# Optimization experiments

Hardware: AMD Instinct MI355X
Metric: run time of the kernel (lower is better)

The kernel has to match this reference:

```python
import jax, jax.numpy as jnp
import numpy as np

B, S, D_IN, D_OUT = 4, 2048, 1024, 1024


def setup_inputs() -> dict:
    key = jax.random.key(0)
    k1, k2, k3, k4 = jax.random.split(key, 4)
    scale = 1.0 / np.sqrt(D_IN)
    return {
        "x": jax.random.normal(k1, (B, S, D_IN), dtype=jnp.float32),
        "W_q": jax.random.normal(k2, (D_OUT, D_IN), dtype=jnp.float32) * scale,
        "W_k": jax.random.normal(k3, (D_OUT, D_IN), dtype=jnp.float32) * scale,
        "W_v": jax.random.normal(k4, (D_OUT, D_IN), dtype=jnp.float32) * scale,
    }


def reference(x, W_q, W_k, W_v):
    # torch nn.Linear: y = x @ W.T (bias=False)
    q = jnp.einsum("bsd,od->bso", x, W_q)
    k = jnp.einsum("bsd,od->bso", x, W_k)
    v = jnp.einsum("bsd,od->bso", x, W_v)
    s = q.shape[1]
    scores = jnp.einsum("bqo,bko->bqk", q, k)  # [B, S, S]
    causal = jnp.triu(jnp.ones((s, s), dtype=bool), k=1)
    scores = jnp.where(causal, -jnp.inf, scores)
    inv_sqrt_d = 1.0 / jnp.sqrt(jnp.asarray(q.shape[-1], scores.dtype))
    attn = jax.nn.softmax(scores * inv_sqrt_d, axis=-1)
    # dropout p=0.0 -> identity (deterministic reference)
    return jnp.einsum("bqk,bko->bqo", attn, v)
```

## Files before the change

### kernel.cpp

```cpp
#include <hip/hip_runtime.h>

typedef unsigned short u16;
typedef __bf16 bf16x8 __attribute__((ext_vector_type(8)));
typedef float f32x4 __attribute__((ext_vector_type(4)));

#define AS1 __attribute__((address_space(1)))
#define AS3 __attribute__((address_space(3)))

__device__ inline u16 f2bf(float f) {
  union { float f; unsigned u; } a; a.f = f;
  unsigned u = a.u;
  return (u16)((u + 0x7fffu + ((u >> 16) & 1u)) >> 16);
}

__global__ __launch_bounds__(256) void cvt_all_kernel(
    const float* __restrict__ x, const float* __restrict__ wq,
    const float* __restrict__ wk, const float* __restrict__ wv,
    u16* __restrict__ xb, u16* __restrict__ wqb,
    u16* __restrict__ wkb, u16* __restrict__ wvb) {
  int bid = blockIdx.x;
  const float* in; u16* out;
  if (bid < 8192) { in = x; out = xb; }
  else if (bid < 9216) { in = wq; out = wqb; bid -= 8192; }
  else if (bid < 10240) { in = wk; out = wkb; bid -= 9216; }
  else { in = wv; out = wvb; bid -= 10240; }
  size_t i = ((size_t)bid * 256 + threadIdx.x) * 4;
  float4 v = *(const float4*)(in + i);
  ushort4 o;
  o.x = f2bf(v.x); o.y = f2bf(v.y); o.z = f2bf(v.z); o.w = f2bf(v.w);
  *(ushort4*)(out + i) = o;
}

template <typename CT, int BN>
__device__ __forceinline__ void gemm_core(
    u16* __restrict__ lds,
    const u16* __restrict__ A, const u16* __restrict__ B, CT* __restrict__ C,
    int nt, int lda, int ldb, int ldc, int m0, int n0) {
  constexpr int ABUF = 16384;
  constexpr int BBUF = BN * 64;
  constexpr int BSW = BN / 64;
  constexpr int NI = BN / 64;

  const int tid = threadIdx.x;
  const int ln = tid & 63, wv = tid >> 6;
  const int wr = wv >> 2, wc = wv & 3;

  auto sweep = [&](const u16* src, int ld, int t, int s, int base) {
    const int c = s * 512 + tid;
    const int row = c >> 3, slot = c & 7;
    const int col = (slot ^ (row & 7)) * 8;
    __builtin_amdgcn_global_load_lds(
        (const AS1 void*)(src + (size_t)row * ld + (size_t)t * 64 + col),
        (AS3 void*)(&lds[base + c * 8]), 16, 0, 0);
  };

  f32x4 acc[8][NI] = {};

#pragma unroll
  for (int s = 0; s < BSW; ++s) sweep(B, ldb, 0, s, 2 * ABUF);
#pragma unroll
  for (int s = 0; s < 4; ++s) sweep(A, lda, 0, s, 0);
  if (nt > 1) {
#pragma unroll
    for (int s = 0; s < BSW; ++s) sweep(B, ldb, 1, s, 2 * ABUF + BBUF);
#pragma unroll
    for (int s = 0; s < 4; ++s) sweep(A, lda, 1, s, ABUF);
    if constexpr (BSW == 4) asm volatile("s_waitcnt vmcnt(8)" ::: "memory");
    else                    asm volatile("s_waitcnt vmcnt(6)" ::: "memory");
  } else {
    asm volatile("s_waitcnt vmcnt(0)" ::: "memory");
  }
  __builtin_amdgcn_s_barrier();

  for (int t = 0; t < nt; ++t) {
    const int p = t & 1;
    const u16* La = &lds[p * ABUF];
    const u16* Lb = &lds[2 * ABUF + p * BBUF];
    bf16x8 bfr[NI][2];
#pragma unroll
    for (int q = 0; q < 4; ++q) {
      if (q == 0) {
        __builtin_amdgcn_sched_barrier(0);
#pragma unroll
        for (int ni = 0; ni < NI; ++ni)
#pragma unroll
          for (int ks = 0; ks < 2; ++ks) {
            const int row = wc * (BN / 4) + ni * 16 + (ln & 15);
            const int kc = ks * 4 + (ln >> 4);
            bfr[ni][ks] = *(const bf16x8*)&Lb[row * 64 + ((kc ^ (row & 7)) << 3)];
          }
      }
      bf16x8 afr[2][2];
#pragma unroll
      for (int mi = 0; mi < 2; ++mi)
#pragma unroll
        for (int ks = 0; ks < 2; ++ks) {
          const int row = wr * 128 + (q * 2 + mi) * 16 + (ln & 15);
          const int kc = ks * 4 + (ln >> 4);
          afr[mi][ks] = *(const bf16x8*)&La[row * 64 + ((kc ^ (row & 7)) << 3)];
        }
      if (q == 0)      { if (t >= 1 && t + 1 < nt) { sweep(A, lda, t + 1, 0, (p ^ 1) * ABUF); sweep(A, lda, t + 1, 1, (p ^ 1) * ABUF); } }
      else if (q == 1) { if (t >= 1 && t + 1 < nt) { sweep(A, lda, t + 1, 2, (p ^ 1) * ABUF); sweep(A, lda, t + 1, 3, (p ^ 1) * ABUF); } }
      else if (q == 2) { if (t + 2 < nt) { sweep(B, ldb, t + 2, 0, 2 * ABUF + p * BBUF); if (BSW == 4) sweep(B, ldb, t + 2, 1, 2 * ABUF + p * BBUF); } }
      else             { if (t + 2 < nt) { if (BSW == 4) { sweep(B, ldb, t + 2, 2, 2 * ABUF + p * BBUF); sweep(B, ldb, t + 2, 3, 2 * ABUF + p * BBUF); } else { sweep(B, ldb, t + 2, 1, 2 * ABUF + p * BBUF); } } }

      __builtin_amdgcn_s_barrier();
      __builtin_amdgcn_s_setprio(1);
#pragma unroll
      for (int mi = 0; mi < 2; ++mi)
#pragma unroll
        for (int ni = 0; ni < NI; ++ni)
#pragma unroll
          for (int ks = 0; ks < 2; ++ks)
            acc[q * 2 + mi][ni] = __builtin_amdgcn_mfma_f32_16x16x32_bf16(
                afr[mi][ks], bfr[ni][ks], acc[q * 2 + mi][ni], 0, 0, 0);
      __builtin_amdgcn_s_setprio(0);
      if (q == 3) {
        if (t + 2 < nt) {
          if constexpr (BSW == 4) asm volatile("s_waitcnt vmcnt(4)" ::: "memory");
          else                    asm volatile("s_waitcnt vmcnt(2)" ::: "memory");
        } else if (t + 1 < nt) {
          asm volatile("s_waitcnt vmcnt(0)" ::: "memory");
        }
      }
      __builtin_amdgcn_s_barrier();
    }
  }

#pragma unroll
  for (int mi = 0; mi < 8; ++mi) {
    const int rbase = m0 + wr * 128 + mi * 16 + (ln >> 4) * 4;
#pragma unroll
    for (int ni = 0; ni < NI; ++ni) {
      const int col = n0 + wc * (BN / 4) + ni * 16 + (ln & 15);
#pragma unroll
      for (int r = 0; r < 4; ++r) {
        const float v = acc[mi][ni][r];
        CT* ptr = &C[(size_t)(rbase + r) * ldc + col];
        if constexpr (sizeof(CT) == 4) *(float*)ptr = v;
        else                           *ptr = f2bf(v);
      }
    }
  }
}

__global__ __launch_bounds__(512, 2) void proj_qk_kernel(
    const u16* __restrict__ xb, const u16* __restrict__ wqb,
    const u16* __restrict__ wkb, u16* __restrict__ Qb, u16* __restrict__ Kb) {
  __shared__ __align__(16) u16 lds[65536];
  const int bid = blockIdx.x;
  const int w = bid >> 7, r = bid & 127;
  const int rb = r >> 2, n0 = (r & 3) * 256;
  const u16* B = w ? wkb : wqb;
  u16* C = w ? Kb : Qb;
  gemm_core<u16, 256>(lds, xb + (size_t)rb * 256 * 1024, B + (size_t)n0 * 1024,
                      C, 16, 1024, 1024, 1024, rb * 256, n0);
}

__global__ __launch_bounds__(512, 2) void qktvt_kernel(
    const u16* __restrict__ Qb, const u16* __restrict__ Kb, float* __restrict__ Sb,
    const u16* __restrict__ wvb, const u16* __restrict__ xb, u16* __restrict__ VTb) {
  __shared__ __align__(16) u16 lds[65536];
  const int bid = blockIdx.x;
  if (bid < 144) {
    const int z = bid / 36, xt = bid % 36;
    int m = 0;
    while ((m + 1) * (m + 2) / 2 <= xt) ++m;
    const int n = xt - m * (m + 1) / 2;
    gemm_core<float, 256>(lds,
        Qb + ((size_t)z * 2048 + m * 256) * 1024,
        Kb + ((size_t)z * 2048 + n * 256) * 1024,
        Sb + (size_t)z * 2048 * 2048,
        16, 1024, 1024, 2048, m * 256, n * 256);
  } else {
    const int j = bid - 144;
    const int z = j / 28, r2 = j % 28, d = r2 / 7, kb = r2 % 7;
    gemm_core<u16, 256>(lds, wvb + (size_t)d * 256 * 1024,
                        xb + (size_t)z * 2048 * 1024 + (size_t)kb * 256 * 1024,
                        VTb + (size_t)z * 1024 * 2048,
                        16, 1024, 1024, 2048, d * 256, kb * 256);
  }
}

__global__ __launch_bounds__(512, 2) void smvtk_kernel(
    float* __restrict__ Sb,
    const u16* __restrict__ wvb, const u16* __restrict__ xb) {
  __shared__ __align__(16) u16 lds[65536];
  const int bid = blockIdx.x;
  const int tid = threadIdx.x;
  if (bid < 64) {
    const int z = bid >> 4, r = bid & 15;
    const int d = r >> 2, kf = (r >> 1) & 1, h = r & 1;
    const u16* A = wvb + (size_t)d * 256 * 1024 + h * 512;
    const u16* B = xb + ((size_t)z * 2048 + 1792 + kf * 128) * 1024 + h * 512;
    const int i = (d * 2 + kf) * 2 + h;
    const int band = i >> 3, coli = i & 7;
    float* C = Sb + (size_t)z * 2048 * 2048 + (size_t)band * 256 * 2048 +
               1024 + coli * 128;
    gemm_core<float, 128>(lds, A, B, C, 8, 1024, 1024, 2048, 0, 0);
    return;
  }
  const int j = bid - 64;
  const int m = 7 - (j >> 6), z = (j >> 4) & 3, s = j & 15;
  const int iters = m + 1;
  const int wvid = tid >> 6, lane = tid & 63;
  float* S0 = Sb + (size_t)z * 2048 * 2048;
  for (int rr = wvid; rr < 16; rr += 8) {
    const int r = m * 256 + s * 16 + rr;
    float* row = S0 + (size_t)r * 2048;
    float vals[8][4];
    float mx = -3.4e38f;
#pragma unroll
    for (int it2 = 0; it2 < 8; ++it2)
      if (it2 < iters) {
        const int idx = it2 * 64 + lane;
        float4 v = ((const float4*)row)[idx];
        const int j0 = idx * 4;
        vals[it2][0] = (j0 <= r) ? v.x * 0.03125f : -3.4e38f;
        vals[it2][1] = (j0 + 1 <= r) ? v.y * 0.03125f : -3.4e38f;
        vals[it2][2] = (j0 + 2 <= r) ? v.z * 0.03125f : -3.4e38f;
        vals[it2][3] = (j0 + 3 <= r) ? v.w * 0.03125f : -3.4e38f;
        mx = fmaxf(mx, fmaxf(fmaxf(vals[it2][0], vals[it2][1]),
                             fmaxf(vals[it2][2], vals[it2][3])));
      }
#pragma unroll
    for (int o = 32; o; o >>= 1) mx = fmaxf(mx, __shfl_xor(mx, o, 64));
    float sum = 0.f;
#pragma unroll
    for (int it2 = 0; it2 < 8; ++it2)
      if (it2 < iters) {
#pragma unroll
        for (int e = 0; e < 4; ++e) {
          const float pp = __expf(vals[it2][e] - mx);
          vals[it2][e] = pp;
          sum += pp;
        }
      }
#pragma unroll
    for (int o = 32; o; o >>= 1) sum += __shfl_xor(sum, o, 64);
    const float rcp = 1.f / sum;
    u16* prow = (u16*)row;
#pragma unroll
    for (int it2 = 0; it2 < 8; ++it2)
      if (it2 < iters) {
        ushort4 o4;
        o4.x = f2bf(vals[it2][0] * rcp);
        o4.y = f2bf(vals[it2][1] * rcp);
        o4.z = f2bf(vals[it2][2] * rcp);
        o4.w = f2bf(vals[it2][3] * rcp);
        ((ushort4*)prow)[it2 * 64 + lane] = o4;
      }
  }
}

__global__ __launch_bounds__(256) void vtfix_kernel(const float* __restrict__ Sb,
                                                    u16* __restrict__ VTb) {
  const int bid = blockIdx.x;
  const int z = bid >> 3, sdk = bid & 7;
  const int d = sdk >> 1, kf = sdk & 1;
  const int i0 = sdk * 2;
  const int band = i0 >> 3, coli = i0 & 7;
  const float* P0 = Sb + (size_t)z * 2048 * 2048 + (size_t)band * 256 * 2048 +
                    1024 + coli * 128;
  const float* P1 = P0 + 128;
  u16* dst = VTb + (size_t)z * 1024 * 2048 + (size_t)d * 256 * 2048 +
             1792 + kf * 128;
  for (int k = threadIdx.x; k < 8192; k += 256) {
    const int r = k >> 5, c4 = (k & 31) << 2;
    float4 a = *(const float4*)(P0 + (size_t)r * 2048 + c4);
    float4 b = *(const float4*)(P1 + (size_t)r * 2048 + c4);
    ushort4 o;
    o.x = f2bf(a.x + b.x); o.y = f2bf(a.y + b.y);
    o.z = f2bf(a.z + b.z); o.w = f2bf(a.w + b.w);
    *(ushort4*)(dst + (size_t)r * 2048 + c4) = o;
  }
}

__constant__ signed char CPM[16] = {5,5,7,7,7,6,4,4,6,6,3,3,1,2,2,0};
__constant__ signed char CPK[16] = {0,12,0,11,22,0,0,10,10,19,0,8,0,0,6,0};
__constant__ signed char CPN[16] = {12,12,11,11,10,10,10,10,9,9,8,8,8,6,6,4};
__constant__ signed char CPS[16] = {0,1,0,1,2,0,0,1,1,2,0,1,0,0,1,0};

__global__ __launch_bounds__(512, 2) void pv_kernel(
    const u16* __restrict__ P, const u16* __restrict__ VTb,
    float* __restrict__ out, float* __restrict__ Sb) {
  __shared__ __align__(16) u16 lds[65536];
  const int cls = blockIdx.x, n = blockIdx.y;
  const size_t z = blockIdx.z;
  const int m = CPM[cls], k0 = CPK[cls], ntc = CPN[cls], sl = CPS[cls];
  const u16* Ap = P + z * 2048 * 4096 + (size_t)m * 256 * 4096 + (size_t)k0 * 64;
  const u16* Bp = VTb + z * 1024 * 2048 + (size_t)n * 256 * 2048 + (size_t)k0 * 64;
  float* Cp;
  int ldc;
  if (sl == 0) { Cp = out + z * 2048 * 1024; ldc = 1024; }
  else if (sl == 1) { Cp = Sb + z * 2048 * 2048 + 1024; ldc = 2048; }
  else { Cp = Sb + z * 2048 * 2048 + 1024 - (size_t)1536 * 2048; ldc = 2048; }
  gemm_core<float, 256>(lds, Ap, Bp, Cp, ntc, 4096, 2048, ldc, m * 256, n * 256);
}

__global__ __launch_bounds__(256) void reduce_kernel(float* __restrict__ out,
                                                     const float* __restrict__ Sb) {
  const int j = blockIdx.x;
  const int m = 2 + (j >> 5), z = (j >> 3) & 3, s = j & 7;
  float* ob = out + (size_t)z * 2048 * 1024;
  const float* s1 = Sb + (size_t)z * 2048 * 2048 + 1024;
  const float* s2 = s1 - (size_t)1536 * 2048;
  const int r0 = m * 256 + s * 32;
  for (int k = threadIdx.x; k < 32 * 256; k += 256) {
    const int rr = r0 + (k >> 8), cc = k & 255;
    float4 o = ((float4*)(ob + (size_t)rr * 1024))[cc];
    float4 a = ((const float4*)(s1 + (size_t)rr * 2048))[cc];
    o.x += a.x; o.y += a.y; o.z += a.z; o.w += a.w;
    if (m >= 6) {
      float4 b = ((const float4*)(s2 + (size_t)rr * 2048))[cc];
      o.x += b.x; o.y += b.y; o.z += b.z; o.w += b.w;
    }
    ((float4*)(ob + (size_t)rr * 1024))[cc] = o;
  }
}

extern "C" void kernel_launch(void* const* d_in, const int* in_sizes, int n_in,
                              void* d_out, int out_size, void* d_ws, size_t ws_size,
                              hipStream_t stream) {
  const float* x  = (const float*)d_in[0];
  const float* Wq = (const float*)d_in[1];
  const float* Wk = (const float*)d_in[2];
  const float* Wv = (const float*)d_in[3];
  float* out = (float*)d_out;

  char* ws = (char*)d_ws;
  u16* xb   = (u16*)(ws);
  u16* wqb  = (u16*)(ws + (16ul << 20));
  u16* wkb  = (u16*)(ws + (18ul << 20));
  u16* wvb  = (u16*)(ws + (20ul << 20));
  u16* Qb   = (u16*)(ws + (22ul << 20));
  u16* Kb   = (u16*)(ws + (38ul << 20));
  u16* VTb  = (u16*)(ws + (54ul << 20));
  float* Sb = (float*)(ws + (70ul << 20));

  cvt_all_kernel<<<11264, 256, 0, stream>>>(x, Wq, Wk, Wv, xb, wqb, wkb, wvb);

  proj_qk_kernel<<<256, 512, 0, stream>>>(xb, wqb, wkb, Qb, Kb);

  qktvt_kernel<<<256, 512, 0, stream>>>(Qb, Kb, Sb, wvb, xb, VTb);

  smvtk_kernel<<<576, 512, 0, stream>>>(Sb, wvb, xb);

  vtfix_kernel<<<32, 256, 0, stream>>>(Sb, VTb);

  pv_kernel<<<dim3(16, 4, 4), 512, 0, stream>>>((const u16*)Sb, VTb, out, Sb);

  reduce_kernel<<<192, 256, 0, stream>>>(out, Sb);
}
```

Before: 172.7 us.

## Store attention scores in bf16 and move split-K partials to a separate buffer

The QK^T GEMM now writes its scores as bf16 instead of fp32, and the softmax pass reads and writes those bf16 values in place, which halves score-matrix traffic. The partial sums for the V^T tail and the PV split-K results move from scratch space inside the score buffer to a dedicated buffer R with new addressing. The qktvt block order is also interleaved so that score tiles and V^T tiles mix across the grid. The cost is that scores are rounded to bf16 before softmax, which lowers precision.

```diff
diff --git a/kernel.cpp b/kernel.cpp
--- a/kernel.cpp
+++ b/kernel.cpp
@@ -1,6 +1,7 @@
 #include <hip/hip_runtime.h>
 
 typedef unsigned short u16;
+typedef unsigned int u32;
 typedef __bf16 bf16x8 __attribute__((ext_vector_type(8)));
 typedef float f32x4 __attribute__((ext_vector_type(4)));
 
@@ -11,6 +12,9 @@
   union { float f; unsigned u; } a; a.f = f;
   unsigned u = a.u;
   return (u16)((u + 0x7fffu + ((u >> 16) & 1u)) >> 16);
+}
+__device__ inline float bf2f(u16 h) {
+  union { unsigned u; float f; } a; a.u = ((u32)h) << 16; return a.f;
 }
 
 __global__ __launch_bounds__(256) void cvt_all_kernel(
@@ -158,22 +162,23 @@
 }
 
 __global__ __launch_bounds__(512, 2) void qktvt_kernel(
-    const u16* __restrict__ Qb, const u16* __restrict__ Kb, float* __restrict__ Sb,
+    const u16* __restrict__ Qb, const u16* __restrict__ Kb, u16* __restrict__ Sb16,
     const u16* __restrict__ wvb, const u16* __restrict__ xb, u16* __restrict__ VTb) {
   __shared__ __align__(16) u16 lds[65536];
   const int bid = blockIdx.x;
-  if (bid < 144) {
-    const int z = bid / 36, xt = bid % 36;
+  const int item = (bid & 7) * 32 + (bid >> 3);
+  if (item < 144) {
+    const int z = item / 36, xt = item % 36;
     int m = 0;
     while ((m + 1) * (m + 2) / 2 <= xt) ++m;
     const int n = xt - m * (m + 1) / 2;
-    gemm_core<float, 256>(lds,
+    gemm_core<u16, 256>(lds,
         Qb + ((size_t)z * 2048 + m * 256) * 1024,
         Kb + ((size_t)z * 2048 + n * 256) * 1024,
-        Sb + (size_t)z * 2048 * 2048,
+        Sb16 + (size_t)z * 2048 * 2048,
         16, 1024, 1024, 2048, m * 256, n * 256);
   } else {
-    const int j = bid - 144;
+    const int j = item - 144;
     const int z = j / 28, r2 = j % 28, d = r2 / 7, kb = r2 % 7;
     gemm_core<u16, 256>(lds, wvb + (size_t)d * 256 * 1024,
                         xb + (size_t)z * 2048 * 1024 + (size_t)kb * 256 * 1024,
@@ -182,55 +187,53 @@
   }
 }
 
-__global__ __launch_bounds__(512, 2) void smvtk_kernel(
-    float* __restrict__ Sb,
+__global__ __launch_bounds__(512, 2) void smvt_kernel(
+    u16* __restrict__ Sb16, float* __restrict__ R,
     const u16* __restrict__ wvb, const u16* __restrict__ xb) {
   __shared__ __align__(16) u16 lds[65536];
   const int bid = blockIdx.x;
   const int tid = threadIdx.x;
-  if (bid < 64) {
-    const int z = bid >> 4, r = bid & 15;
-    const int d = r >> 2, kf = (r >> 1) & 1, h = r & 1;
+  if (bid < 32) {
+    const int z = bid >> 3, r = bid & 7;
+    const int d = r >> 1, h = r & 1;
     const u16* A = wvb + (size_t)d * 256 * 1024 + h * 512;
-    const u16* B = xb + ((size_t)z * 2048 + 1792 + kf * 128) * 1024 + h * 512;
-    const int i = (d * 2 + kf) * 2 + h;
-    const int band = i >> 3, coli = i & 7;
-    float* C = Sb + (size_t)z * 2048 * 2048 + (size_t)band * 256 * 2048 +
-               1024 + coli * 128;
-    gemm_core<float, 128>(lds, A, B, C, 8, 1024, 1024, 2048, 0, 0);
+    const u16* B = xb + ((size_t)z * 2048 + 1792) * 1024 + h * 512;
+    float* C = R + (size_t)z * 2097152 + 1572864 + (d * 2 + h) * 65536;
+    gemm_core<float, 256>(lds, A, B, C, 8, 1024, 1024, 256, 0, 0);
     return;
   }
-  const int j = bid - 64;
+  const int j = bid - 32;
   const int m = 7 - (j >> 6), z = (j >> 4) & 3, s = j & 15;
-  const int iters = m + 1;
+  const int iters = (m + 2) >> 1;
   const int wvid = tid >> 6, lane = tid & 63;
-  float* S0 = Sb + (size_t)z * 2048 * 2048;
+  u16* S0 = Sb16 + (size_t)z * 2048 * 2048;
   for (int rr = wvid; rr < 16; rr += 8) {
     const int r = m * 256 + s * 16 + rr;
-    float* row = S0 + (size_t)r * 2048;
-    float vals[8][4];
+    u16* row = S0 + (size_t)r * 2048;
+    float vals[4][8];
     float mx = -3.4e38f;
 #pragma unroll
-    for (int it2 = 0; it2 < 8; ++it2)
+    for (int it2 = 0; it2 < 4; ++it2)
       if (it2 < iters) {
-        const int idx = it2 * 64 + lane;
-        float4 v = ((const float4*)row)[idx];
-        const int j0 = idx * 4;
-        vals[it2][0] = (j0 <= r) ? v.x * 0.03125f : -3.4e38f;
-        vals[it2][1] = (j0 + 1 <= r) ? v.y * 0.03125f : -3.4e38f;
-        vals[it2][2] = (j0 + 2 <= r) ? v.z * 0.03125f : -3.4e38f;
-        vals[it2][3] = (j0 + 3 <= r) ? v.w * 0.03125f : -3.4e38f;
-        mx = fmaxf(mx, fmaxf(fmaxf(vals[it2][0], vals[it2][1]),
-                             fmaxf(vals[it2][2], vals[it2][3])));
+        const int idx8 = it2 * 512 + lane * 8;
+        uint4 w = *(const uint4*)(row + idx8);
+        const u32 ws[4] = {w.x, w.y, w.z, w.w};
+#pragma unroll
+        for (int e = 0; e < 8; ++e) {
+          const u16 hb = (u16)(ws[e >> 1] >> ((e & 1) * 16));
+          const float xv = bf2f(hb) * 0.03125f;
+          vals[it2][e] = (idx8 + e <= r) ? xv : -3.4e38f;
+          mx = fmaxf(mx, vals[it2][e]);
+        }
       }
 #pragma unroll
     for (int o = 32; o; o >>= 1) mx = fmaxf(mx, __shfl_xor(mx, o, 64));
     float sum = 0.f;
 #pragma unroll
-    for (int it2 = 0; it2 < 8; ++it2)
+    for (int it2 = 0; it2 < 4; ++it2)
       if (it2 < iters) {
 #pragma unroll
-        for (int e = 0; e < 4; ++e) {
+        for (int e = 0; e < 8; ++e) {
           const float pp = __expf(vals[it2][e] - mx);
           vals[it2][e] = pp;
           sum += pp;
@@ -239,40 +242,40 @@
 #pragma unroll
     for (int o = 32; o; o >>= 1) sum += __shfl_xor(sum, o, 64);
     const float rcp = 1.f / sum;
-    u16* prow = (u16*)row;
-#pragma unroll
-    for (int it2 = 0; it2 < 8; ++it2)
+#pragma unroll
+    for (int it2 = 0; it2 < 4; ++it2)
       if (it2 < iters) {
-        ushort4 o4;
-        o4.x = f2bf(vals[it2][0] * rcp);
-        o4.y = f2bf(vals[it2][1] * rcp);
-        o4.z = f2bf(vals[it2][2] * rcp);
-        o4.w = f2bf(vals[it2][3] * rcp);
-        ((ushort4*)prow)[it2 * 64 + lane] = o4;
-      }
-  }
-}
-
-__global__ __launch_bounds__(256) void vtfix_kernel(const float* __restrict__ Sb,
+        const int idx8 = it2 * 512 + lane * 8;
+        uint4 w;
+        u32 wo[4];
+#pragma unroll
+        for (int e2 = 0; e2 < 4; ++e2) {
+          const u16 lo = f2bf(vals[it2][e2 * 2] * rcp);
+          const u16 hi = f2bf(vals[it2][e2 * 2 + 1] * rcp);
+          wo[e2] = (u32)lo | ((u32)hi << 16);
+        }
+        w.x = wo[0]; w.y = wo[1]; w.z = wo[2]; w.w = wo[3];
+        *(uint4*)(row + idx8) = w;
+      }
+  }
+}
+
+__global__ __launch_bounds__(256) void vtfix_kernel(const float* __restrict__ R,
                                                     u16* __restrict__ VTb) {
   const int bid = blockIdx.x;
-  const int z = bid >> 3, sdk = bid & 7;
-  const int d = sdk >> 1, kf = sdk & 1;
-  const int i0 = sdk * 2;
-  const int band = i0 >> 3, coli = i0 & 7;
-  const float* P0 = Sb + (size_t)z * 2048 * 2048 + (size_t)band * 256 * 2048 +
-                    1024 + coli * 128;
-  const float* P1 = P0 + 128;
-  u16* dst = VTb + (size_t)z * 1024 * 2048 + (size_t)d * 256 * 2048 +
-             1792 + kf * 128;
-  for (int k = threadIdx.x; k < 8192; k += 256) {
-    const int r = k >> 5, c4 = (k & 31) << 2;
-    float4 a = *(const float4*)(P0 + (size_t)r * 2048 + c4);
-    float4 b = *(const float4*)(P1 + (size_t)r * 2048 + c4);
+  const int z = bid >> 3, q = bid & 7;
+  const int d = q >> 1, rh = q & 1;
+  const float* P0 = R + (size_t)z * 2097152 + 1572864 + (d * 2 + 0) * 65536;
+  const float* P1 = R + (size_t)z * 2097152 + 1572864 + (d * 2 + 1) * 65536;
+  for (int k = threadIdx.x; k < 128 * 64; k += 256) {
+    const int dp = rh * 128 + (k >> 6), c4 = (k & 63) * 4;
+    float4 a = *(const float4*)(P0 + (size_t)dp * 256 + c4);
+    float4 b = *(const float4*)(P1 + (size_t)dp * 256 + c4);
     ushort4 o;
     o.x = f2bf(a.x + b.x); o.y = f2bf(a.y + b.y);
     o.z = f2bf(a.z + b.z); o.w = f2bf(a.w + b.w);
-    *(ushort4*)(dst + (size_t)r * 2048 + c4) = o;
+    *(ushort4*)(VTb + (size_t)z * 1024 * 2048 + (size_t)(d * 256 + dp) * 2048 +
+                1792 + c4) = o;
   }
 }
 
@@ -283,36 +286,35 @@
 
 __global__ __launch_bounds__(512, 2) void pv_kernel(
     const u16* __restrict__ P, const u16* __restrict__ VTb,
-    float* __restrict__ out, float* __restrict__ Sb) {
+    float* __restrict__ out, float* __restrict__ R) {
   __shared__ __align__(16) u16 lds[65536];
   const int cls = blockIdx.x, n = blockIdx.y;
   const size_t z = blockIdx.z;
   const int m = CPM[cls], k0 = CPK[cls], ntc = CPN[cls], sl = CPS[cls];
-  const u16* Ap = P + z * 2048 * 4096 + (size_t)m * 256 * 4096 + (size_t)k0 * 64;
+  const u16* Ap = P + z * 2048 * 2048 + (size_t)m * 256 * 2048 + (size_t)k0 * 64;
   const u16* Bp = VTb + z * 1024 * 2048 + (size_t)n * 256 * 2048 + (size_t)k0 * 64;
   float* Cp;
-  int ldc;
-  if (sl == 0) { Cp = out + z * 2048 * 1024; ldc = 1024; }
-  else if (sl == 1) { Cp = Sb + z * 2048 * 2048 + 1024; ldc = 2048; }
-  else { Cp = Sb + z * 2048 * 2048 + 1024 - (size_t)1536 * 2048; ldc = 2048; }
-  gemm_core<float, 256>(lds, Ap, Bp, Cp, ntc, 4096, 2048, ldc, m * 256, n * 256);
+  if (sl == 0)      Cp = out + z * 2048 * 1024;
+  else if (sl == 1) Cp = R + z * 2097152 - (size_t)512 * 1024;
+  else              Cp = R + z * 2097152;
+  gemm_core<float, 256>(lds, Ap, Bp, Cp, ntc, 2048, 2048, 1024, m * 256, n * 256);
 }
 
 __global__ __launch_bounds__(256) void reduce_kernel(float* __restrict__ out,
-                                                     const float* __restrict__ Sb) {
+                                                     const float* __restrict__ R) {
   const int j = blockIdx.x;
   const int m = 2 + (j >> 5), z = (j >> 3) & 3, s = j & 7;
   float* ob = out + (size_t)z * 2048 * 1024;
-  const float* s1 = Sb + (size_t)z * 2048 * 2048 + 1024;
-  const float* s2 = s1 - (size_t)1536 * 2048;
+  const float* s1 = R + (size_t)z * 2097152;
+  const float* s2 = s1 + 1572864;
   const int r0 = m * 256 + s * 32;
   for (int k = threadIdx.x; k < 32 * 256; k += 256) {
     const int rr = r0 + (k >> 8), cc = k & 255;
     float4 o = ((float4*)(ob + (size_t)rr * 1024))[cc];
-    float4 a = ((const float4*)(s1 + (size_t)rr * 2048))[cc];
+    float4 a = ((const float4*)(s1 + (size_t)(rr - 512) * 1024))[cc];
     o.x += a.x; o.y += a.y; o.z += a.z; o.w += a.w;
     if (m >= 6) {
-      float4 b = ((const float4*)(s2 + (size_t)rr * 2048))[cc];
+      float4 b = ((const float4*)(s2 + (size_t)(rr - 1536) * 1024))[cc];
       o.x += b.x; o.y += b.y; o.z += b.z; o.w += b.w;
     }
     ((float4*)(ob + (size_t)rr * 1024))[cc] = o;
@@ -336,19 +338,20 @@
   u16* Qb   = (u16*)(ws + (22ul << 20));
   u16* Kb   = (u16*)(ws + (38ul << 20));
   u16* VTb  = (u16*)(ws + (54ul << 20));
-  float* Sb = (float*)(ws + (70ul << 20));
+  u16* Sb16 = (u16*)(ws + (70ul << 20));
+  float* R  = (float*)(ws + (102ul << 20));
 
   cvt_all_kernel<<<11264, 256, 0, stream>>>(x, Wq, Wk, Wv, xb, wqb, wkb, wvb);
 
   proj_qk_kernel<<<256, 512, 0, stream>>>(xb, wqb, wkb, Qb, Kb);
 
-  qktvt_kernel<<<256, 512, 0, stream>>>(Qb, Kb, Sb, wvb, xb, VTb);
-
-  smvtk_kernel<<<576, 512, 0, stream>>>(Sb, wvb, xb);
-
-  vtfix_kernel<<<32, 256, 0, stream>>>(Sb, VTb);
-
-  pv_kernel<<<dim3(16, 4, 4), 512, 0, stream>>>((const u16*)Sb, VTb, out, Sb);
-
-  reduce_kernel<<<192, 256, 0, stream>>>(out, Sb);
-}
+  qktvt_kernel<<<256, 512, 0, stream>>>(Qb, Kb, Sb16, wvb, xb, VTb);
+
+  smvt_kernel<<<544, 512, 0, stream>>>(Sb16, R, wvb, xb);
+
+  vtfix_kernel<<<32, 256, 0, stream>>>(R, VTb);
+
+  pv_kernel<<<dim3(16, 4, 4), 512, 0, stream>>>(Sb16, VTb, out, R);
+
+  reduce_kernel<<<192, 256, 0, stream>>>(out, R);
+}
```

Measured after the change: 161.0 us. -6.8%, faster.
